# Performance work log

Measured on AMD Instinct MI355X. Metric: run time of the kernel, lower is better.

## Reference

```python
import jax, jax.numpy as jnp
import numpy as np

IOU_THR = 0.8
SCORE_THR = 0.7
INNER_THR = 0.5
EPS = 1e-8


def setup_inputs() -> dict:
    key = jax.random.key(0)
    k1, k2 = jax.random.split(key)
    N, H, W = 1024, 256, 256
    masks = (jax.random.uniform(k1, (N, H, W)) < 0.15).astype(jnp.float32)
    scores = jax.random.uniform(k2, (N,), dtype=jnp.float32)
    return {"masks": masks, "scores": scores}


def reference(masks, scores):
    N = masks.shape[0]
    # sort by score descending (torch: scores.sort(0, descending=True))
    order = jnp.argsort(-scores)
    s = scores[order]
    flat = masks[order].reshape(N, -1).astype(jnp.float32)  # [N, H*W]
    area = jnp.sum(flat, axis=1)                            # [N]

    inter = flat @ flat.T                                   # [N, N]
    union = area[None, :] + area[:, None] - inter
    iou = inter / (union + EPS)
    ratio_i = inter / (area[:, None] + EPS)
    ratio_j = inter / (area[None, :] + EPS)
    vals = 1.0 - ratio_j * ratio_i

    cond1 = (ratio_i < 0.5) & (ratio_j >= 0.85)
    cond2 = (ratio_i >= 0.85) & (ratio_j < 0.5)
    # inner_iou_matrix[cond1] = vals[cond1]
    inner = jnp.where(cond1, vals, 0.0)
    # inner_iou_matrix.T[cond2] = vals[cond2]  =>  inner[j,i] = vals[i,j] where cond2[i,j]
    inner = jnp.where(cond2.T, vals.T, inner)

    triu1 = jnp.triu(jnp.ones((N, N), dtype=bool), k=1)
    tril1 = jnp.tril(jnp.ones((N, N), dtype=bool), k=1)  # note diagonal=1, matches torch.tril(., 1)

    iou_max = jnp.max(jnp.where(triu1, iou, 0.0), axis=0)
    inner_max_u = jnp.max(jnp.where(triu1, inner, 0.0), axis=0)
    inner_max_l = jnp.max(jnp.where(tril1, inner, 0.0), axis=0)

    keep = iou_max <= IOU_THR
    keep_conf = s > SCORE_THR
    # fallback: if no mask passes score threshold, keep top-3 by score
    _, top3 = jax.lax.top_k(s, 3)
    fallback = jnp.zeros((N,), dtype=bool).at[top3].set(True)
    keep_conf = jnp.where(jnp.any(keep_conf), keep_conf, fallback)

    keep = keep & keep_conf & (inner_max_u <= 1.0 - INNER_THR) & (inner_max_l <= 1.0 - INNER_THR)
    # torch returns idx[keep] (dynamic shape); we return (order, keep) which is equivalent info
    return order, keep
```

## Files before the change

### kernel.cpp

```cpp
#include <hip/hip_runtime.h>


#define N_MASKS 1024
#define HW 65536
#define WPR 2048
#define NT 8
#define NPAIRS 36
#define KQ 16

typedef float vfloat4 __attribute__((ext_vector_type(4)));
typedef int v4i __attribute__((ext_vector_type(4)));
typedef int v16i __attribute__((ext_vector_type(16)));

__device__ __forceinline__ void tile_from_pair(int p, int& I, int& J) {
    int rem = p, i = 0;
    while (rem >= NT - i) { rem -= NT - i; ++i; }
    I = i; J = i + rem;
}

__global__ __launch_bounds__(128) void sort_kernel(const float* __restrict__ scores,
                                                   int* __restrict__ order,
                                                   float* __restrict__ ssort,
                                                   int* __restrict__ out_order,
                                                   float* __restrict__ area,
                                                   unsigned* __restrict__ ioumax,
                                                   unsigned* __restrict__ innu,
                                                   unsigned* __restrict__ innl) {
    __shared__ float s[N_MASKS];
    const int t = threadIdx.x;
    for (int k = t; k < N_MASKS; k += 128) s[k] = scores[k];
    __syncthreads();
    const int i = blockIdx.x * 128 + t;
    const float si = s[i];
    int rank = 0;
    #pragma unroll 8
    for (int j = 0; j < N_MASKS; ++j) {
        const float sj = s[j];
        rank += (int)((sj > si) || (sj == si && j < i));
    }
    order[rank] = i;
    ssort[rank] = si;
    out_order[rank] = i;
    area[i] = 0.0f;
    ioumax[i] = 0u; innu[i] = 0u; innl[i] = 0u;
}

__global__ __launch_bounds__(256, 4) void pack_kernel(const float* __restrict__ masks,
                                                      const int* __restrict__ order,
                                                      unsigned* __restrict__ packed,
                                                      float* __restrict__ area) {
    const int b = blockIdx.x;
    const int r = b >> 2, q = b & 3;
    const int src = order[r];
    const vfloat4* __restrict__ row = (const vfloat4*)(masks + (size_t)src * HW) + q * 4096;
    unsigned* __restrict__ prow = packed + (size_t)r * WPR + q * 512;
    const int t = threadIdx.x;

    vfloat4 f[16];
    #pragma unroll
    for (int k = 0; k < 16; ++k)
        f[k] = __builtin_nontemporal_load(row + k * 256 + t);

    unsigned w0 = 0u, w1 = 0u;
    #pragma unroll
    for (int k = 0; k < 8; ++k) {
        const unsigned nib0 = (unsigned)(f[k][0] != 0.0f)        | ((unsigned)(f[k][1] != 0.0f) << 1)
                            | ((unsigned)(f[k][2] != 0.0f) << 2) | ((unsigned)(f[k][3] != 0.0f) << 3);
        w0 |= nib0 << (k * 4);
        const unsigned nib1 = (unsigned)(f[k + 8][0] != 0.0f)        | ((unsigned)(f[k + 8][1] != 0.0f) << 1)
                            | ((unsigned)(f[k + 8][2] != 0.0f) << 2) | ((unsigned)(f[k + 8][3] != 0.0f) << 3);
        w1 |= nib1 << (k * 4);
    }
    prow[t] = w0;
    prow[256 + t] = w1;

    int cnt = __builtin_popcount(w0) + __builtin_popcount(w1);
    for (int off = 32; off > 0; off >>= 1) cnt += __shfl_down(cnt, off, 64);
    __shared__ int red[4];
    const int lane = t & 63, w = t >> 6;
    if (lane == 0) red[w] = cnt;
    __syncthreads();
    if (t == 0) atomicAdd(area + r, (float)(red[0] + red[1] + red[2] + red[3]));
}

__global__ __launch_bounds__(256, 2) void pair_kernel(const unsigned* __restrict__ packed,
                                                      int* __restrict__ partial) {
    __shared__ __align__(16) unsigned lA[128 * 64];
    __shared__ __align__(16) unsigned lB[128 * 64];

    const int p = blockIdx.x, kq = blockIdx.y;
    int I, J; tile_from_pair(p, I, J);
    const int A0 = I * 128, B0 = J * 128;
    const int t = threadIdx.x;
    const int wave = t >> 6, lane = t & 63, half = lane >> 5, lr = lane & 31;
    const int wr = (wave >> 1) * 64, wc = (wave & 1) * 64;
    const int srow = t & 127, shalf = t >> 7;

    v16i acc[2][2];
    #pragma unroll
    for (int i = 0; i < 2; ++i)
        #pragma unroll
        for (int j = 0; j < 2; ++j)
            #pragma unroll
            for (int r = 0; r < 16; ++r) acc[i][j][r] = 0;

    const int sw = srow & 15;

    #pragma unroll 1
    for (int ch = 0; ch < 16; ++ch) {
        __syncthreads();
        const uint4 wa = *(const uint4*)(packed + (size_t)(A0 + srow) * WPR + kq * 128 + ch * 8 + shalf * 4);
        const uint4 wb = *(const uint4*)(packed + (size_t)(B0 + srow) * WPR + kq * 128 + ch * 8 + shalf * 4);
        #pragma unroll
        for (int w = 0; w < 4; ++w) {
            const unsigned a = (w == 0) ? wa.x : (w == 1) ? wa.y : (w == 2) ? wa.z : wa.w;
            const unsigned b = (w == 0) ? wb.x : (w == 1) ? wb.y : (w == 2) ? wb.z : wb.w;
            const int wcid = shalf * 4 + w;
            uint4 lo, hi;
            lo.x = ((a         & 0xFu) * 0x00204081u) & 0x01010101u;
            lo.y = (((a >> 4)  & 0xFu) * 0x00204081u) & 0x01010101u;
            lo.z = (((a >> 8)  & 0xFu) * 0x00204081u) & 0x01010101u;
            lo.w = (((a >> 12) & 0xFu) * 0x00204081u) & 0x01010101u;
            hi.x = (((a >> 16) & 0xFu) * 0x00204081u) & 0x01010101u;
            hi.y = (((a >> 20) & 0xFu) * 0x00204081u) & 0x01010101u;
            hi.z = (((a >> 24) & 0xFu) * 0x00204081u) & 0x01010101u;
            hi.w = (((a >> 28) & 0xFu) * 0x00204081u) & 0x01010101u;
            *(uint4*)(lA + srow * 64 + (((wcid * 2)     ^ sw) << 2)) = lo;
            *(uint4*)(lA + srow * 64 + (((wcid * 2 + 1) ^ sw) << 2)) = hi;
            lo.x = ((b         & 0xFu) * 0x00204081u) & 0x01010101u;
            lo.y = (((b >> 4)  & 0xFu) * 0x00204081u) & 0x01010101u;
            lo.z = (((b >> 8)  & 0xFu) * 0x00204081u) & 0x01010101u;
            lo.w = (((b >> 12) & 0xFu) * 0x00204081u) & 0x01010101u;
            hi.x = (((b >> 16) & 0xFu) * 0x00204081u) & 0x01010101u;
            hi.y = (((b >> 20) & 0xFu) * 0x00204081u) & 0x01010101u;
            hi.z = (((b >> 24) & 0xFu) * 0x00204081u) & 0x01010101u;
            hi.w = (((b >> 28) & 0xFu) * 0x00204081u) & 0x01010101u;
            *(uint4*)(lB + srow * 64 + (((wcid * 2)     ^ sw) << 2)) = lo;
            *(uint4*)(lB + srow * 64 + (((wcid * 2 + 1) ^ sw) << 2)) = hi;
        }
        __syncthreads();

        #pragma unroll
        for (int kk = 0; kk < 8; ++kk) {
            const int phys = ((kk * 2 + half) ^ (lr & 15)) << 2;
            const v4i a0 = *(const v4i*)(lA + (wr + lr) * 64 + phys);
            const v4i a1 = *(const v4i*)(lA + (wr + 32 + lr) * 64 + phys);
            const v4i b0 = *(const v4i*)(lB + (wc + lr) * 64 + phys);
            const v4i b1 = *(const v4i*)(lB + (wc + 32 + lr) * 64 + phys);
            acc[0][0] = __builtin_amdgcn_mfma_i32_32x32x32_i8(a0, b0, acc[0][0], 0, 0, 0);
            acc[0][1] = __builtin_amdgcn_mfma_i32_32x32x32_i8(a0, b1, acc[0][1], 0, 0, 0);
            acc[1][0] = __builtin_amdgcn_mfma_i32_32x32x32_i8(a1, b0, acc[1][0], 0, 0, 0);
            acc[1][1] = __builtin_amdgcn_mfma_i32_32x32x32_i8(a1, b1, acc[1][1], 0, 0, 0);
        }
    }

    int* __restrict__ outp = partial + ((size_t)kq * NPAIRS + p) * 16384;
    #pragma unroll
    for (int i = 0; i < 2; ++i)
        #pragma unroll
        for (int j = 0; j < 2; ++j)
            #pragma unroll
            for (int reg = 0; reg < 16; ++reg) {
                const int m = wr + i * 32 + (reg & 3) + 8 * (reg >> 2) + 4 * half;
                const int n = wc + j * 32 + lr;
                outp[m * 128 + n] = acc[i][j][reg];
            }
}

__global__ __launch_bounds__(256) void combine_kernel(const unsigned* __restrict__ partial,
                                                      const float* __restrict__ area,
                                                      unsigned* __restrict__ ioumax,
                                                      unsigned* __restrict__ innu,
                                                      unsigned* __restrict__ innl) {
    __shared__ unsigned redI[128], redU[128], redLB[128], redLA[8];
    __shared__ float aB[128];

    const int p = blockIdx.x, rg = blockIdx.y;
    int I, J; tile_from_pair(p, I, J);
    const int A0 = I * 128, B0 = J * 128;
    const int t = threadIdx.x;
    if (t < 128) { redI[t] = 0u; redU[t] = 0u; redLB[t] = 0u; aB[t] = area[B0 + t]; }
    if (t < 8) redLA[t] = 0u;
    __syncthreads();

    const int row = rg * 8 + (t >> 5);
    const int col = (t & 31) * 4;
    const int a = A0 + row;
    const float fa = area[a];

    unsigned sx = 0, sy = 0, sz = 0, sw = 0;
    #pragma unroll
    for (int kq = 0; kq < KQ; ++kq) {
        const uint4 v = *(const uint4*)(partial + ((size_t)kq * NPAIRS + p) * 16384 + row * 128 + col);
        sx += v.x; sy += v.y; sz += v.z; sw += v.w;
    }
    const unsigned sums[4] = { sx, sy, sz, sw };

    float mLA = 0.0f;
    #pragma unroll
    for (int j = 0; j < 4; ++j) {
        const int b = B0 + col + j;
        if (a > b) continue;
        const float inter = (float)sums[j];
        const float fb = aB[col + j];
        const float uni = (fb + fa) - inter;
        const float iou = inter / (uni + 1e-8f);
        const float ra = inter / (fa + 1e-8f);
        const float rb = inter / (fb + 1e-8f);
        const float v = __fsub_rn(1.0f, __fmul_rn(rb, ra));
        const float iab = (ra < 0.5f && rb >= 0.85f) ? v : 0.0f;
        const float iba = (rb < 0.5f && ra >= 0.85f) ? v : 0.0f;
        if (a < b) {
            atomicMax(&redI[col + j], __float_as_uint(iou));
            atomicMax(&redU[col + j], __float_as_uint(iab));
            mLA = fmaxf(mLA, iba);
        }
        if (a == b - 1) atomicMax(&redLB[col + j], __float_as_uint(iab));
    }
    atomicMax(&redLA[t >> 5], __float_as_uint(mLA));
    __syncthreads();
    if (t < 128) {
        atomicMax(&ioumax[B0 + t], redI[t]);
        atomicMax(&innu[B0 + t], redU[t]);
        atomicMax(&innl[B0 + t], redLB[t]);
    }
    if (t < 8) atomicMax(&innl[A0 + rg * 8 + t], redLA[t]);
}

__global__ __launch_bounds__(256) void keep_kernel(const float* __restrict__ ssort,
                                                   const unsigned* __restrict__ ioumax,
                                                   const unsigned* __restrict__ innu,
                                                   const unsigned* __restrict__ innl,
                                                   int* __restrict__ out_keep) {
    const int r = blockIdx.x * 256 + threadIdx.x;
    const float s0 = ssort[0];
    const bool conf = (s0 > 0.7f) ? (ssort[r] > 0.7f) : (r < 3);
    const bool keep = (__uint_as_float(ioumax[r]) <= 0.8f) && conf &&
                      (__uint_as_float(innu[r]) <= 0.5f) &&
                      (__uint_as_float(innl[r]) <= 0.5f);
    out_keep[r] = keep ? 1 : 0;
}

extern "C" void kernel_launch(void* const* d_in, const int* in_sizes, int n_in,
                              void* d_out, int out_size, void* d_ws, size_t ws_size,
                              hipStream_t stream) {
    const float* masks  = (const float*)d_in[0];
    const float* scores = (const float*)d_in[1];
    int* out = (int*)d_out;

    unsigned* packed  = (unsigned*)d_ws;
    unsigned* partial = packed + (size_t)N_MASKS * WPR;
    unsigned* tail    = partial + (size_t)KQ * NPAIRS * 16384;
    int*      order   = (int*)tail;
    float*    ssort   = (float*)(order + N_MASKS);
    float*    area    = (float*)(ssort + N_MASKS);
    unsigned* ioumax  = (unsigned*)(area + N_MASKS);
    unsigned* innu    = ioumax + N_MASKS;
    unsigned* innl    = innu + N_MASKS;

    sort_kernel<<<8, 128, 0, stream>>>(scores, order, ssort, out, area, ioumax, innu, innl);
    pack_kernel<<<4096, 256, 0, stream>>>(masks, order, packed, area);
    pair_kernel<<<dim3(NPAIRS, KQ), 256, 0, stream>>>(packed, (int*)partial);
    combine_kernel<<<dim3(NPAIRS, KQ), 256, 0, stream>>>(partial, area, ioumax, innu, innl);
    keep_kernel<<<4, 256, 0, stream>>>(ssort, ioumax, innu, innl, out + N_MASKS);
}
```

Baseline: 437.5 us.

## Expand packed bits directly into MFMA registers, dropping LDS staging

The pair kernel no longer stages expanded int8 masks in shared memory. Each lane now loads its own packed bit-words from global memory and expands them in registers straight into MFMA operands, which removes the barriers and LDS traffic. The occupancy hint rises to 3 blocks per CU, and on diagonal tiles one wave exits early because its block is redundant there. In exchange each word is loaded and expanded redundantly by several waves, so global/L2 traffic and VALU expansion work per MFMA go up.

```diff
diff --git a/kernel.cpp b/kernel.cpp
--- a/kernel.cpp
+++ b/kernel.cpp
@@ -16,6 +16,15 @@
     int rem = p, i = 0;
     while (rem >= NT - i) { rem -= NT - i; ++i; }
     I = i; J = i + rem;
+}
+
+__device__ __forceinline__ v4i expand16(unsigned word, int sh) {
+    v4i r;
+    r[0] = (int)((((word >> (sh + 0))  & 0xFu) * 0x00204081u) & 0x01010101u);
+    r[1] = (int)((((word >> (sh + 4))  & 0xFu) * 0x00204081u) & 0x01010101u);
+    r[2] = (int)((((word >> (sh + 8))  & 0xFu) * 0x00204081u) & 0x01010101u);
+    r[3] = (int)((((word >> (sh + 12)) & 0xFu) * 0x00204081u) & 0x01010101u);
+    return r;
 }
 
 __global__ __launch_bounds__(128) void sort_kernel(const float* __restrict__ scores,
@@ -83,18 +92,22 @@
     if (t == 0) atomicAdd(area + r, (float)(red[0] + red[1] + red[2] + red[3]));
 }
 
-__global__ __launch_bounds__(256, 2) void pair_kernel(const unsigned* __restrict__ packed,
+__global__ __launch_bounds__(256, 3) void pair_kernel(const unsigned* __restrict__ packed,
                                                       int* __restrict__ partial) {
-    __shared__ __align__(16) unsigned lA[128 * 64];
-    __shared__ __align__(16) unsigned lB[128 * 64];
-
     const int p = blockIdx.x, kq = blockIdx.y;
     int I, J; tile_from_pair(p, I, J);
     const int A0 = I * 128, B0 = J * 128;
     const int t = threadIdx.x;
     const int wave = t >> 6, lane = t & 63, half = lane >> 5, lr = lane & 31;
     const int wr = (wave >> 1) * 64, wc = (wave & 1) * 64;
-    const int srow = t & 127, shalf = t >> 7;
+
+    if (I == J && wave == 2) return;
+
+    const unsigned* __restrict__ rowA0 = packed + (size_t)(A0 + wr + lr) * WPR + kq * 128;
+    const unsigned* __restrict__ rowA1 = rowA0 + 32 * WPR;
+    const unsigned* __restrict__ rowB0 = packed + (size_t)(B0 + wc + lr) * WPR + kq * 128;
+    const unsigned* __restrict__ rowB1 = rowB0 + 32 * WPR;
+    const int sh = half * 16;
 
     v16i acc[2][2];
     #pragma unroll
@@ -104,49 +117,22 @@
             #pragma unroll
             for (int r = 0; r < 16; ++r) acc[i][j][r] = 0;
 
-    const int sw = srow & 15;
-
-    #pragma unroll 1
-    for (int ch = 0; ch < 16; ++ch) {
-        __syncthreads();
-        const uint4 wa = *(const uint4*)(packed + (size_t)(A0 + srow) * WPR + kq * 128 + ch * 8 + shalf * 4);
-        const uint4 wb = *(const uint4*)(packed + (size_t)(B0 + srow) * WPR + kq * 128 + ch * 8 + shalf * 4);
+    #pragma unroll 2
+    for (int g = 0; g < 32; ++g) {
+        const uint4 wa0 = *(const uint4*)(rowA0 + g * 4);
+        const uint4 wa1 = *(const uint4*)(rowA1 + g * 4);
+        const uint4 wb0 = *(const uint4*)(rowB0 + g * 4);
+        const uint4 wb1 = *(const uint4*)(rowB1 + g * 4);
+        const unsigned a0w[4] = { wa0.x, wa0.y, wa0.z, wa0.w };
+        const unsigned a1w[4] = { wa1.x, wa1.y, wa1.z, wa1.w };
+        const unsigned b0w[4] = { wb0.x, wb0.y, wb0.z, wb0.w };
+        const unsigned b1w[4] = { wb1.x, wb1.y, wb1.z, wb1.w };
         #pragma unroll
         for (int w = 0; w < 4; ++w) {
-            const unsigned a = (w == 0) ? wa.x : (w == 1) ? wa.y : (w == 2) ? wa.z : wa.w;
-            const unsigned b = (w == 0) ? wb.x : (w == 1) ? wb.y : (w == 2) ? wb.z : wb.w;
-            const int wcid = shalf * 4 + w;
-            uint4 lo, hi;
-            lo.x = ((a         & 0xFu) * 0x00204081u) & 0x01010101u;
-            lo.y = (((a >> 4)  & 0xFu) * 0x00204081u) & 0x01010101u;
-            lo.z = (((a >> 8)  & 0xFu) * 0x00204081u) & 0x01010101u;
-            lo.w = (((a >> 12) & 0xFu) * 0x00204081u) & 0x01010101u;
-            hi.x = (((a >> 16) & 0xFu) * 0x00204081u) & 0x01010101u;
-            hi.y = (((a >> 20) & 0xFu) * 0x00204081u) & 0x01010101u;
-            hi.z = (((a >> 24) & 0xFu) * 0x00204081u) & 0x01010101u;
-            hi.w = (((a >> 28) & 0xFu) * 0x00204081u) & 0x01010101u;
-            *(uint4*)(lA + srow * 64 + (((wcid * 2)     ^ sw) << 2)) = lo;
-            *(uint4*)(lA + srow * 64 + (((wcid * 2 + 1) ^ sw) << 2)) = hi;
-            lo.x = ((b         & 0xFu) * 0x00204081u) & 0x01010101u;
-            lo.y = (((b >> 4)  & 0xFu) * 0x00204081u) & 0x01010101u;
-            lo.z = (((b >> 8)  & 0xFu) * 0x00204081u) & 0x01010101u;
-            lo.w = (((b >> 12) & 0xFu) * 0x00204081u) & 0x01010101u;
-            hi.x = (((b >> 16) & 0xFu) * 0x00204081u) & 0x01010101u;
-            hi.y = (((b >> 20) & 0xFu) * 0x00204081u) & 0x01010101u;
-            hi.z = (((b >> 24) & 0xFu) * 0x00204081u) & 0x01010101u;
-            hi.w = (((b >> 28) & 0xFu) * 0x00204081u) & 0x01010101u;
-            *(uint4*)(lB + srow * 64 + (((wcid * 2)     ^ sw) << 2)) = lo;
-            *(uint4*)(lB + srow * 64 + (((wcid * 2 + 1) ^ sw) << 2)) = hi;
-        }
-        __syncthreads();
-
-        #pragma unroll
-        for (int kk = 0; kk < 8; ++kk) {
-            const int phys = ((kk * 2 + half) ^ (lr & 15)) << 2;
-            const v4i a0 = *(const v4i*)(lA + (wr + lr) * 64 + phys);
-            const v4i a1 = *(const v4i*)(lA + (wr + 32 + lr) * 64 + phys);
-            const v4i b0 = *(const v4i*)(lB + (wc + lr) * 64 + phys);
-            const v4i b1 = *(const v4i*)(lB + (wc + 32 + lr) * 64 + phys);
+            const v4i a0 = expand16(a0w[w], sh);
+            const v4i a1 = expand16(a1w[w], sh);
+            const v4i b0 = expand16(b0w[w], sh);
+            const v4i b1 = expand16(b1w[w], sh);
             acc[0][0] = __builtin_amdgcn_mfma_i32_32x32x32_i8(a0, b0, acc[0][0], 0, 0, 0);
             acc[0][1] = __builtin_amdgcn_mfma_i32_32x32x32_i8(a0, b1, acc[0][1], 0, 0, 0);
             acc[1][0] = __builtin_amdgcn_mfma_i32_32x32x32_i8(a1, b0, acc[1][0], 0, 0, 0);
```

Measured after the change: 429.5 us (median of 2 runs). About the same (-1.8%).
